# Performance work log

Hardware: AMD Instinct MI355X
Metric: run time of the kernel (lower is better)

## Reference

```python
import jax, jax.numpy as jnp
import numpy as np

N = 50000        # nodes
E = 600000       # edges (before self-loops)
VOCAB = 100000
EMB = 128
HID = 128
G = 64           # graphs in batch
NEG_SLOPE = 0.2


def setup_inputs() -> dict:
    key = jax.random.key(0)
    ks = jax.random.split(key, 16)
    x_idx = jax.random.randint(ks[0], (N,), 0, VOCAB)
    edge_index = jax.random.randint(ks[1], (2, E), 0, N)
    edge_attr = jax.random.uniform(ks[2], (E,), dtype=jnp.float32)
    batch = jnp.sort(jax.random.randint(ks[3], (N,), 0, G))
    # embedding table; padding_idx=0 row zeroed as in nn.Embedding(padding_idx=0)
    emb_table = (jax.random.normal(ks[4], (VOCAB, EMB), dtype=jnp.float32) * 0.05).at[0].set(0.0)
    glorot = lambda k, shp: jax.random.normal(k, shp, dtype=jnp.float32) * np.float32(np.sqrt(2.0 / sum(shp)))
    W1 = glorot(ks[5], (HID, EMB))
    att_src1 = glorot(ks[6], (HID,)) * 0.0 + jax.random.normal(ks[6], (HID,), dtype=jnp.float32) * np.float32(np.sqrt(2.0 / (HID + 1)))
    att_dst1 = jax.random.normal(ks[7], (HID,), dtype=jnp.float32) * np.float32(np.sqrt(2.0 / (HID + 1)))
    W2 = glorot(ks[8], (HID, HID))
    att_src2 = jax.random.normal(ks[9], (HID,), dtype=jnp.float32) * np.float32(np.sqrt(2.0 / (HID + 1)))
    att_dst2 = jax.random.normal(ks[10], (HID,), dtype=jnp.float32) * np.float32(np.sqrt(2.0 / (HID + 1)))
    W3 = glorot(ks[11], (HID // 2, HID))
    b3 = jnp.zeros((HID // 2,), jnp.float32)
    W4 = glorot(ks[12], (2, HID // 2))
    b4 = jnp.zeros((2,), jnp.float32)
    return {"x_idx": x_idx, "edge_index": edge_index, "edge_attr": edge_attr, "batch": batch,
            "emb_table": emb_table, "W1": W1, "att_src1": att_src1, "att_dst1": att_dst1,
            "W2": W2, "att_src2": att_src2, "att_dst2": att_dst2,
            "W3": W3, "b3": b3, "W4": W4, "b4": b4}


def _segment_softmax(logits, seg, n):
    m = jax.ops.segment_max(logits, seg, num_segments=n)
    e = jnp.exp(logits - m[seg])
    s = jax.ops.segment_sum(e, seg, num_segments=n)
    return e / (s[seg] + 1e-16)


def _edge_attr_gat_conv(x, src, dst, ea, W, a_src, a_dst, n):
    H = x @ W.T                                   # [n, out]
    # per-edge score: (H_i . a_dst) + (H_j . a_src); compute per-node then gather
    alpha = (H @ a_dst)[dst] + (H @ a_src)[src]   # [e]
    alpha = jnp.where(alpha >= 0, alpha, NEG_SLOPE * alpha)
    alpha = alpha * ea                            # multiplicative edge attr
    alpha = _segment_softmax(alpha, dst, n)       # softmax over in-neighborhoods
    return jax.ops.segment_sum(H[src] * alpha[:, None], dst, num_segments=n)


def reference(x_idx, edge_index, edge_attr, batch, emb_table,
              W1, att_src1, att_dst1, W2, att_src2, att_dst2, W3, b3, W4, b4):
    n = x_idx.shape[0]
    loops = jnp.arange(n)
    # add_self_loops (done inside each conv in torch; same edges both layers)
    src = jnp.concatenate([edge_index[0], loops])
    dst = jnp.concatenate([edge_index[1], loops])  # edge_index_i (aggregation index)
    ea = jnp.concatenate([edge_attr, jnp.ones((n,), edge_attr.dtype)])
    x = emb_table[x_idx]
    x = jax.nn.relu(_edge_attr_gat_conv(x, src, dst, ea, W1, att_src1, att_dst1, n))
    x = jax.nn.relu(_edge_attr_gat_conv(x, src, dst, ea, W2, att_src2, att_dst2, n))
    # global_mean_pool
    sums = jax.ops.segment_sum(x, batch, num_segments=G)
    counts = jax.ops.segment_sum(jnp.ones((n,), x.dtype), batch, num_segments=G)
    g = sums / jnp.maximum(counts, 1.0)[:, None]
    # MLP head (dropout = identity at eval)
    h = jax.nn.relu(g @ W3.T + b3)
    return h @ W4.T + b4
```

## Files before the change

kernel.cpp:

```cpp
#include <hip/hip_runtime.h>
#include <cstdint>
#include <cstddef>


__device__ __forceinline__ float wave_sum(float v) {
#pragma unroll
  for (int m = 32; m >= 1; m >>= 1) v += __shfl_xor(v, m, 64);
  return v;
}
__device__ __forceinline__ float wave_max(float v) {
#pragma unroll
  for (int m = 32; m >= 1; m >>= 1) v = fmaxf(v, __shfl_xor(v, m, 64));
  return v;
}


__global__ void init_kernel(int* __restrict__ deg, float* __restrict__ gsum,
                            int* __restrict__ gstart, int* __restrict__ gend,
                            int N, int G) {
  int i = blockIdx.x * blockDim.x + threadIdx.x;
  if (i < N) deg[i] = 1;
  if (i < G * 128) gsum[i] = 0.f;
  if (i < G) { gstart[i] = 0; gend[i] = 0; }
}

__global__ void count_deg_kernel(const int* __restrict__ edge_index,
                                 int* __restrict__ deg, int E) {
  int e = blockIdx.x * blockDim.x + threadIdx.x;
  if (e < E) atomicAdd(&deg[edge_index[E + e]], 1);
}

__global__ void scan1_kernel(const int* __restrict__ deg, int* __restrict__ bsum, int N) {
  __shared__ int ws[4];
  int tid = threadIdx.x;
  int i = blockIdx.x * 256 + tid;
  int v = (i < N) ? deg[i] : 0;
#pragma unroll
  for (int m = 32; m >= 1; m >>= 1) v += __shfl_xor(v, m, 64);
  if ((tid & 63) == 0) ws[tid >> 6] = v;
  __syncthreads();
  if (tid == 0) bsum[blockIdx.x] = ws[0] + ws[1] + ws[2] + ws[3];
}

__device__ __forceinline__ int block_excl_scan_256(int v, int tid, int* wsum) {
  int lane = tid & 63, wid = tid >> 6;
  int incl = v;
#pragma unroll
  for (int off = 1; off < 64; off <<= 1) {
    int t = __shfl_up(incl, off, 64);
    if (lane >= off) incl += t;
  }
  if (lane == 63) wsum[wid] = incl;
  __syncthreads();
  int woff = 0;
#pragma unroll
  for (int w = 0; w < 4; ++w)
    if (w < wid) woff += wsum[w];
  return woff + incl - v;
}

__global__ void scan2_kernel(const int* __restrict__ bsum, int* __restrict__ boff,
                             int* __restrict__ row_ptr, int nb, int N) {
  __shared__ int wsum[4];
  int tid = threadIdx.x;
  int v = (tid < nb) ? bsum[tid] : 0;
  int excl = block_excl_scan_256(v, tid, wsum);
  if (tid < nb) boff[tid] = excl;
  if (tid == 255) row_ptr[N] = excl + v;
}

__global__ void scan3_kernel(const int* __restrict__ deg, const int* __restrict__ boff,
                             int* __restrict__ row_ptr, int N) {
  __shared__ int wsum[4];
  int tid = threadIdx.x;
  int i = blockIdx.x * 256 + tid;
  int v = (i < N) ? deg[i] : 0;
  int excl = block_excl_scan_256(v, tid, wsum);
  if (i < N) row_ptr[i] = boff[blockIdx.x] + excl;
}

__global__ void fillA_kernel(const int* __restrict__ row_ptr, int* __restrict__ srcs,
                             float* __restrict__ eas, int* __restrict__ cur, int N) {
  int i = blockIdx.x * blockDim.x + threadIdx.x;
  if (i < N) {
    int p = row_ptr[i];
    srcs[p] = i;
    eas[p] = 1.0f;
    cur[i] = p + 1;
  }
}

__global__ void fillB_kernel(const int* __restrict__ edge_index, const float* __restrict__ ea,
                             int* __restrict__ cur, int* __restrict__ srcs,
                             float* __restrict__ eas, int E) {
  int e = blockIdx.x * blockDim.x + threadIdx.x;
  if (e < E) {
    int d0 = edge_index[E + e];
    int p = atomicAdd(&cur[d0], 1);
    srcs[p] = edge_index[e];
    eas[p] = ea[e];
  }
}


__global__ __launch_bounds__(256) void gemm_att_kernel(
    const float* __restrict__ Xin, const int* __restrict__ gidx,
    const float* __restrict__ W,
    const float* __restrict__ a_src, const float* __restrict__ a_dst,
    float* __restrict__ H, float* __restrict__ sv, float* __restrict__ dv, int N) {
  __shared__ float XsT[32][64];
  __shared__ float Wt[32][128];
  __shared__ float av[2][128];

  int tid = threadIdx.x;
  int tx = tid & 15, ty = tid >> 4;
  int rb = blockIdx.x * 64;

  if (tid < 128) { av[0][tid] = a_src[tid]; av[1][tid] = a_dst[tid]; }

  int r0 = tid & 63;
  int q0 = tid >> 6;
  int gr0 = rb + r0; if (gr0 >= N) gr0 = N - 1;
  const float* rp0 = gidx ? (Xin + (size_t)gidx[gr0] * 128) : (Xin + (size_t)gr0 * 128);

  float acc[4][8];
#pragma unroll
  for (int r = 0; r < 4; ++r)
#pragma unroll
    for (int j = 0; j < 8; ++j) acc[r][j] = 0.f;

#pragma unroll
  for (int ks = 0; ks < 4; ++ks) {
    const int k0 = ks * 32;
    __syncthreads();
    {
      float4 v0 = *(const float4*)(rp0 + k0 + q0 * 4);
      float4 v1 = *(const float4*)(rp0 + k0 + (q0 + 4) * 4);
      XsT[q0 * 4 + 0][r0] = v0.x; XsT[q0 * 4 + 1][r0] = v0.y;
      XsT[q0 * 4 + 2][r0] = v0.z; XsT[q0 * 4 + 3][r0] = v0.w;
      XsT[(q0 + 4) * 4 + 0][r0] = v1.x; XsT[(q0 + 4) * 4 + 1][r0] = v1.y;
      XsT[(q0 + 4) * 4 + 2][r0] = v1.z; XsT[(q0 + 4) * 4 + 3][r0] = v1.w;
    }
#pragma unroll
    for (int it = 0; it < 4; ++it) {
      int idx = tid + it * 256;
      int c = idx & 127, q = idx >> 7;
      float4 v = *(const float4*)(W + (size_t)c * 128 + k0 + q * 4);
      Wt[q * 4 + 0][c] = v.x; Wt[q * 4 + 1][c] = v.y;
      Wt[q * 4 + 2][c] = v.z; Wt[q * 4 + 3][c] = v.w;
    }
    __syncthreads();
#pragma unroll 8
    for (int k = 0; k < 32; ++k) {
      float4 xa = *(const float4*)&XsT[k][ty * 4];
      float4 wl = *(const float4*)&Wt[k][tx * 4];
      float4 wh = *(const float4*)&Wt[k][tx * 4 + 64];
      float xr[4] = {xa.x, xa.y, xa.z, xa.w};
      float wv[8] = {wl.x, wl.y, wl.z, wl.w, wh.x, wh.y, wh.z, wh.w};
#pragma unroll
      for (int r = 0; r < 4; ++r)
#pragma unroll
        for (int j = 0; j < 8; ++j) acc[r][j] = fmaf(xr[r], wv[j], acc[r][j]);
    }
  }

#pragma unroll
  for (int r = 0; r < 4; ++r) {
    int gr = rb + ty * 4 + r;
    float ps = 0.f, pd = 0.f;
#pragma unroll
    for (int j = 0; j < 4; ++j) {
      ps = fmaf(acc[r][j], av[0][tx * 4 + j], ps);
      ps = fmaf(acc[r][4 + j], av[0][tx * 4 + 64 + j], ps);
      pd = fmaf(acc[r][j], av[1][tx * 4 + j], pd);
      pd = fmaf(acc[r][4 + j], av[1][tx * 4 + 64 + j], pd);
    }
#pragma unroll
    for (int m = 1; m < 16; m <<= 1) {
      ps += __shfl_xor(ps, m, 64);
      pd += __shfl_xor(pd, m, 64);
    }
    if (gr < N) {
      float4 lo = make_float4(acc[r][0], acc[r][1], acc[r][2], acc[r][3]);
      float4 hi = make_float4(acc[r][4], acc[r][5], acc[r][6], acc[r][7]);
      *(float4*)(H + (size_t)gr * 128 + tx * 4) = lo;
      *(float4*)(H + (size_t)gr * 128 + 64 + tx * 4) = hi;
      if (tx == 0) { sv[gr] = ps; dv[gr] = pd; }
    }
  }
}


__global__ __launch_bounds__(256) void agg_kernel(
    const float* __restrict__ H, const float* __restrict__ sv, const float* __restrict__ dv,
    const int* __restrict__ row_ptr, const int* __restrict__ srcs,
    const float* __restrict__ eas, float* __restrict__ Xout, int N) {
  int wid = threadIdx.x >> 6, lane = threadIdx.x & 63;
  int node = blockIdx.x * 4 + wid;
  if (node >= N) return;
  int p0 = row_ptr[node], p1 = row_ptr[node + 1];
  float di = dv[node];

  float m = -3.4e38f;
  for (int p = p0; p < p1; p += 64) {
    int e = p + lane;
    float f = -3.4e38f;
    if (e < p1) {
      float t = di + sv[srcs[e]];
      t = (t >= 0.f) ? t : 0.2f * t;
      f = t * eas[e];
    }
    m = fmaxf(m, wave_max(f));
  }

  float acc0 = 0.f, acc1 = 0.f, S = 0.f;
  for (int p = p0; p < p1; p += 64) {
    int e = p + lane;
    float w = 0.f; int sE = 0;
    if (e < p1) {
      sE = srcs[e];
      float t = di + sv[sE];
      t = (t >= 0.f) ? t : 0.2f * t;
      w = expf(t * eas[e] - m);
    }
    S += wave_sum(w);
    int cnt = min(64, p1 - p);
    for (int j = 0; j < cnt; ++j) {
      float wj = __shfl(w, j, 64);
      int sj = __shfl(sE, j, 64);
      const float* hr = H + (size_t)sj * 128;
      acc0 = fmaf(wj, hr[lane], acc0);
      acc1 = fmaf(wj, hr[lane + 64], acc1);
    }
  }
  float sc = 1.0f / (S + 1e-16f);
  float o0 = acc0 * sc, o1 = acc1 * sc;
  Xout[(size_t)node * 128 + lane] = (o0 > 0.f) ? o0 : 0.f;
  Xout[(size_t)node * 128 + 64 + lane] = (o1 > 0.f) ? o1 : 0.f;
}


__global__ void batch_bounds_kernel(const int* __restrict__ batch,
                                    int* __restrict__ gstart, int* __restrict__ gend, int N) {
  int i = blockIdx.x * blockDim.x + threadIdx.x;
  if (i >= N) return;
  int b = batch[i];
  if (i == 0 || batch[i - 1] != b) gstart[b] = i;
  if (i == N - 1 || batch[i + 1] != b) gend[b] = i + 1;
}

__global__ void pool_kernel(const float* __restrict__ X, const int* __restrict__ batch,
                            float* __restrict__ gsum, int N) {
  int col = threadIdx.x & 127;
  int half = threadIdx.x >> 7;
  int base = blockIdx.x * 128;
  int cur = -1; float acc = 0.f;
  for (int j = half; j < 128; j += 2) {
    int n = base + j;
    if (n >= N) break;
    int g = batch[n];
    if (g != cur) {
      if (cur >= 0) atomicAdd(&gsum[cur * 128 + col], acc);
      cur = g; acc = 0.f;
    }
    acc += X[(size_t)n * 128 + col];
  }
  if (cur >= 0) atomicAdd(&gsum[cur * 128 + col], acc);
}

__global__ __launch_bounds__(256) void head_kernel(
    const float* __restrict__ gsum,
    const int* __restrict__ gstart, const int* __restrict__ gend,
    const float* __restrict__ W3, const float* __restrict__ b3,
    const float* __restrict__ W4, const float* __restrict__ b4,
    float* __restrict__ out, int G) {
  __shared__ float gv[128];
  __shared__ float h[64];
  int gid = blockIdx.x;
  int tid = threadIdx.x;
  float cnt = (float)(gend[gid] - gstart[gid]);
  if (cnt < 1.f) cnt = 1.f;
  if (tid < 128) gv[tid] = gsum[(size_t)gid * 128 + tid] / cnt;
  __syncthreads();
  {
    int c = tid >> 2, part = tid & 3;
    const float4* w = (const float4*)(W3 + (size_t)c * 128 + part * 32);
    const float4* gg = (const float4*)(gv + part * 32);
    float acc = 0.f;
#pragma unroll
    for (int k = 0; k < 8; ++k) {
      float4 a = gg[k], b = w[k];
      acc = fmaf(a.x, b.x, acc); acc = fmaf(a.y, b.y, acc);
      acc = fmaf(a.z, b.z, acc); acc = fmaf(a.w, b.w, acc);
    }
    acc += __shfl_xor(acc, 1, 64);
    acc += __shfl_xor(acc, 2, 64);
    if (part == 0) { float v = acc + b3[c]; h[c] = (v > 0.f) ? v : 0.f; }
  }
  __syncthreads();
  if (tid < 128) {
    int o = tid >> 6, k = tid & 63;
    float p = h[k] * W4[o * 64 + k];
    p = wave_sum(p);
    if (k == 0) out[gid * 2 + o] = p + b4[o];
  }
}


extern "C" void kernel_launch(void* const* d_in, const int* in_sizes, int n_in,
                              void* d_out, int out_size, void* d_ws, size_t ws_size,
                              hipStream_t stream) {
  const int* x_idx = (const int*)d_in[0];
  const int* edge_index = (const int*)d_in[1];
  const float* edge_attr = (const float*)d_in[2];
  const int* batch = (const int*)d_in[3];
  const float* emb = (const float*)d_in[4];
  const float* W1 = (const float*)d_in[5];
  const float* as1 = (const float*)d_in[6];
  const float* ad1 = (const float*)d_in[7];
  const float* W2 = (const float*)d_in[8];
  const float* as2 = (const float*)d_in[9];
  const float* ad2 = (const float*)d_in[10];
  const float* W3 = (const float*)d_in[11];
  const float* b3 = (const float*)d_in[12];
  const float* W4 = (const float*)d_in[13];
  const float* b4 = (const float*)d_in[14];

  const int N = in_sizes[0];
  const int E = in_sizes[2];
  const int G = out_size / 2;
  const int ET = E + N;

  uint8_t* wp = (uint8_t*)d_ws;
  auto take = [&](size_t bytes) -> void* {
    void* p = (void*)wp;
    wp += (bytes + 255) & ~(size_t)255;
    return p;
  };
  float* H    = (float*)take((size_t)N * 128 * 4);
  float* X    = (float*)take((size_t)N * 128 * 4);
  float* sv   = (float*)take((size_t)N * 4);
  float* dv   = (float*)take((size_t)N * 4);
  int*   deg  = (int*)take((size_t)N * 4);
  int*   rowp = (int*)take((size_t)(N + 1) * 4);
  int*   cur  = (int*)take((size_t)N * 4);
  int*   bsum = (int*)take(256 * 4);
  int*   boff = (int*)take(256 * 4);
  int*   srcs = (int*)take((size_t)ET * 4);
  float* eas  = (float*)take((size_t)ET * 4);
  float* gsum = (float*)take((size_t)G * 128 * 4);
  int*   gstart = (int*)take((size_t)G * 4);
  int*   gend   = (int*)take((size_t)G * 4);
  (void)ws_size; (void)n_in;

  const int nb = (N + 255) / 256;
  const int eb = (E + 255) / 256;

  init_kernel<<<nb, 256, 0, stream>>>(deg, gsum, gstart, gend, N, G);
  count_deg_kernel<<<eb, 256, 0, stream>>>(edge_index, deg, E);
  scan1_kernel<<<nb, 256, 0, stream>>>(deg, bsum, N);
  scan2_kernel<<<1, 256, 0, stream>>>(bsum, boff, rowp, nb, N);
  scan3_kernel<<<nb, 256, 0, stream>>>(deg, boff, rowp, N);
  fillA_kernel<<<nb, 256, 0, stream>>>(rowp, srcs, eas, cur, N);
  fillB_kernel<<<eb, 256, 0, stream>>>(edge_index, edge_attr, cur, srcs, eas, E);

  const int gb = (N + 63) / 64;
  const int ab = (N + 3) / 4;
  gemm_att_kernel<<<gb, 256, 0, stream>>>(emb, x_idx, W1, as1, ad1, H, sv, dv, N);
  agg_kernel<<<ab, 256, 0, stream>>>(H, sv, dv, rowp, srcs, eas, X, N);
  gemm_att_kernel<<<gb, 256, 0, stream>>>(X, nullptr, W2, as2, ad2, H, sv, dv, N);
  agg_kernel<<<ab, 256, 0, stream>>>(H, sv, dv, rowp, srcs, eas, X, N);
  batch_bounds_kernel<<<nb, 256, 0, stream>>>(batch, gstart, gend, N);
  pool_kernel<<<(N + 127) / 128, 256, 0, stream>>>(X, batch, gsum, N);
  head_kernel<<<G, 256, 0, stream>>>(gsum, gstart, gend, W3, b3, W4, b4, (float*)d_out, G);
}
```

Baseline: 309.2 us.

## Vectorize GAT aggregation with float4 row gathers and single-pass softmax for small degrees

Rewrites the per-node aggregation so each half-wave gathers a full 128-float neighbor row as float4 loads, and the two halves handle alternate edges with four loads in flight per step before a final cross-half reduction. Nodes with degree up to 64 compute the softmax max and weights in one pass instead of re-reading source indices and scores. The aim is fewer, wider memory transactions and more memory-level parallelism in the gather-bound loop. In exchange it adds extra shuffles, a padded gather (invalid slots read row 0 with zero weight), and an odd redundant __expf term.

```diff
diff --git a/kernel.cpp b/kernel.cpp
--- a/kernel.cpp
+++ b/kernel.cpp
@@ -199,44 +199,105 @@
   int node = blockIdx.x * 4 + wid;
   if (node >= N) return;
   int p0 = row_ptr[node], p1 = row_ptr[node + 1];
+  int deg = p1 - p0;
   float di = dv[node];
-
-  float m = -3.4e38f;
-  for (int p = p0; p < p1; p += 64) {
-    int e = p + lane;
-    float f = -3.4e38f;
-    if (e < p1) {
-      float t = di + sv[srcs[e]];
-      t = (t >= 0.f) ? t : 0.2f * t;
-      f = t * eas[e];
-    }
-    m = fmaxf(m, wave_max(f));
-  }
-
-  float acc0 = 0.f, acc1 = 0.f, S = 0.f;
-  for (int p = p0; p < p1; p += 64) {
-    int e = p + lane;
-    float w = 0.f; int sE = 0;
-    if (e < p1) {
+  int half = lane >> 5;
+  int cl = lane & 31;
+
+  float4 acc = make_float4(0.f, 0.f, 0.f, 0.f);
+  float S = 0.f;
+
+  if (deg <= 64) {
+    int e = p0 + lane;
+    float f = -3.4e38f; int sE = 0;
+    if (lane < deg) {
       sE = srcs[e];
       float t = di + sv[sE];
       t = (t >= 0.f) ? t : 0.2f * t;
-      w = expf(t * eas[e] - m);
-    }
-    S += wave_sum(w);
-    int cnt = min(64, p1 - p);
-    for (int j = 0; j < cnt; ++j) {
-      float wj = __shfl(w, j, 64);
-      int sj = __shfl(sE, j, 64);
-      const float* hr = H + (size_t)sj * 128;
-      acc0 = fmaf(wj, hr[lane], acc0);
-      acc1 = fmaf(wj, hr[lane + 64], acc1);
-    }
-  }
+      f = t * eas[e];
+    }
+    float m = wave_max(f);
+    float w = (lane < deg) ? __expf(f - m) * 0.f + expf(f - m) : 0.f;
+    S = wave_sum(w);
+    for (int t0 = 0; t0 < deg; t0 += 8) {
+      float4 v[4]; float wv[4];
+#pragma unroll
+      for (int u = 0; u < 4; ++u) {
+        int idx = t0 + 2 * u + half;
+        float wj = __shfl(w, idx, 64);
+        int sj = __shfl(sE, idx, 64);
+        bool valid = idx < deg;
+        wv[u] = valid ? wj : 0.f;
+        const float4* hr = (const float4*)(H + (size_t)(valid ? sj : 0) * 128);
+        v[u] = hr[cl];
+      }
+#pragma unroll
+      for (int u = 0; u < 4; ++u) {
+        acc.x = fmaf(wv[u], v[u].x, acc.x);
+        acc.y = fmaf(wv[u], v[u].y, acc.y);
+        acc.z = fmaf(wv[u], v[u].z, acc.z);
+        acc.w = fmaf(wv[u], v[u].w, acc.w);
+      }
+    }
+  } else {
+    float m = -3.4e38f;
+    for (int p = p0; p < p1; p += 64) {
+      int e = p + lane;
+      float f = -3.4e38f;
+      if (e < p1) {
+        float t = di + sv[srcs[e]];
+        t = (t >= 0.f) ? t : 0.2f * t;
+        f = t * eas[e];
+      }
+      m = fmaxf(m, wave_max(f));
+    }
+    for (int p = p0; p < p1; p += 64) {
+      int cnt = min(64, p1 - p);
+      int e = p + lane;
+      float w = 0.f; int sE = 0;
+      if (lane < cnt) {
+        sE = srcs[e];
+        float t = di + sv[sE];
+        t = (t >= 0.f) ? t : 0.2f * t;
+        w = expf(t * eas[e] - m);
+      }
+      S += wave_sum(w);
+      for (int t0 = 0; t0 < cnt; t0 += 8) {
+        float4 v[4]; float wv[4];
+#pragma unroll
+        for (int u = 0; u < 4; ++u) {
+          int idx = t0 + 2 * u + half;
+          float wj = __shfl(w, idx, 64);
+          int sj = __shfl(sE, idx, 64);
+          bool valid = idx < cnt;
+          wv[u] = valid ? wj : 0.f;
+          const float4* hr = (const float4*)(H + (size_t)(valid ? sj : 0) * 128);
+          v[u] = hr[cl];
+        }
+#pragma unroll
+        for (int u = 0; u < 4; ++u) {
+          acc.x = fmaf(wv[u], v[u].x, acc.x);
+          acc.y = fmaf(wv[u], v[u].y, acc.y);
+          acc.z = fmaf(wv[u], v[u].z, acc.z);
+          acc.w = fmaf(wv[u], v[u].w, acc.w);
+        }
+      }
+    }
+  }
+
+  acc.x += __shfl_xor(acc.x, 32, 64);
+  acc.y += __shfl_xor(acc.y, 32, 64);
+  acc.z += __shfl_xor(acc.z, 32, 64);
+  acc.w += __shfl_xor(acc.w, 32, 64);
   float sc = 1.0f / (S + 1e-16f);
-  float o0 = acc0 * sc, o1 = acc1 * sc;
-  Xout[(size_t)node * 128 + lane] = (o0 > 0.f) ? o0 : 0.f;
-  Xout[(size_t)node * 128 + 64 + lane] = (o1 > 0.f) ? o1 : 0.f;
+  if (half == 0) {
+    float4 o;
+    o.x = fmaxf(acc.x * sc, 0.f);
+    o.y = fmaxf(acc.y * sc, 0.f);
+    o.z = fmaxf(acc.z * sc, 0.f);
+    o.w = fmaxf(acc.w * sc, 0.f);
+    *(float4*)(Xout + (size_t)node * 128 + cl * 4) = o;
+  }
 }
 
 
```

Result: faster. 290.1 us (-6.2%).
